# Kernel optimization log

Hardware: AMD Instinct MI355X
Metric: run time of the kernel (lower is better)

Reference implementation:

```python
import jax, jax.numpy as jnp
import numpy as np

N = 50000
E_RAND = 800000
IN_DIM, HIDDEN, OUT_DIM, HEADS = 256, 32, 40, 4


def glorot(key, fan_in, fan_out, shape):
    r = np.sqrt(6.0 / (fan_in + fan_out))
    return jax.random.uniform(key, shape, jnp.float32, -r, r)


def setup_inputs() -> dict:
    key = jax.random.key(0)
    ks = jax.random.split(key, 10)
    x = jax.random.normal(ks[0], (N, IN_DIM), jnp.float32)
    # random edges with src != dst, then append self loops (remove+add_self_loops semantics)
    s = jax.random.randint(ks[1], (E_RAND,), 0, N, jnp.int32)
    d = (s + 1 + jax.random.randint(ks[2], (E_RAND,), 0, N - 1, jnp.int32)) % N
    loops = jnp.arange(N, dtype=jnp.int32)
    src = jnp.concatenate([s, loops])
    dst = jnp.concatenate([d, loops])
    lin1 = glorot(ks[3], IN_DIM, HEADS * HIDDEN, (IN_DIM, HEADS * HIDDEN))
    att_q1 = glorot(ks[4], HEADS, HIDDEN, (1, HEADS, HIDDEN))
    att_v1 = glorot(ks[5], HEADS, HIDDEN, (1, HEADS, HIDDEN))
    bias1 = jnp.zeros((HEADS * HIDDEN,), jnp.float32)
    lin2 = glorot(ks[6], HEADS * HIDDEN, HEADS * OUT_DIM, (HEADS * HIDDEN, HEADS * OUT_DIM))
    att_q2 = glorot(ks[7], HEADS, OUT_DIM, (1, HEADS, OUT_DIM))
    att_v2 = glorot(ks[8], HEADS, OUT_DIM, (1, HEADS, OUT_DIM))
    bias2 = jnp.zeros((OUT_DIM,), jnp.float32)
    return {"x": x, "src": src, "dst": dst,
            "lin1": lin1, "att_q1": att_q1, "att_v1": att_v1, "bias1": bias1,
            "lin2": lin2, "att_q2": att_q2, "att_v2": att_v2, "bias2": bias2}


def segment_softmax(e, seg, n):
    # e: [E, H]; softmax grouped by target node seg
    m = jax.ops.segment_max(e, seg, num_segments=n)  # [N, H]
    ex = jnp.exp(e - m[seg])
    s = jax.ops.segment_sum(ex, seg, num_segments=n)
    return ex / (s[seg] + 1e-16)


def ood_gat_conv(x, src, dst, lin, att_q, att_v, bias, concat):
    n = x.shape[0]
    H, C = att_q.shape[1], att_q.shape[2]
    xh = (x @ lin).reshape(n, H, C)                     # [N, H, C]
    alpha = jnp.sum(xh * att_q, axis=-1)                # [N, H]
    sa = jax.nn.sigmoid(alpha)
    w_alpha = 1.0 - jnp.abs(sa[dst] - sa[src])          # [E, H]
    w_beta = jnp.sum(att_v * jax.nn.leaky_relu(xh[dst] + xh[src]), axis=-1)  # [E, H]
    w = segment_softmax(w_alpha * w_beta, dst, n)       # [E, H]
    out = jax.ops.segment_sum(xh[src] * w[..., None], dst, num_segments=n)  # [N, H, C]
    out = out.reshape(n, H * C) if concat else out.mean(axis=1)
    return out + bias


def reference(x, src, dst, lin1, att_q1, att_v1, bias1, lin2, att_q2, att_v2, bias2):
    h = ood_gat_conv(x, src, dst, lin1, att_q1, att_v1, bias1, concat=True)
    h = jax.nn.elu(h)
    out = ood_gat_conv(h, src, dst, lin2, att_q2, att_v2, bias2, concat=False)
    return out
```

## Files before the change

kernel.cpp:

```cpp
#include <hip/hip_runtime.h>
#include <hip/hip_fp16.h>

#define HEADS 4

typedef _Float16 v2h __attribute__((ext_vector_type(2)));

__device__ __forceinline__ float4 ldh4(const __half* p) {
    const uint2 u = *(const uint2*)p;
    const float2 a = __half22float2(*(const __half2*)&u.x);
    const float2 b = __half22float2(*(const __half2*)&u.y);
    return make_float4(a.x, a.y, b.x, b.y);
}

__device__ __forceinline__ __half2 habs2_(__half2 x) {
    unsigned u = *reinterpret_cast<unsigned*>(&x) & 0x7FFF7FFFu;
    return *reinterpret_cast<__half2*>(&u);
}

__device__ __forceinline__ float fdot2_(__half2 a, __half2 b, float c) {
    return __builtin_amdgcn_fdot2(*(v2h*)&a, *(v2h*)&b, c, false);
}

template <int BN, bool AHALF>
__device__ __forceinline__ void gemm_alpha_body(
    const void* __restrict__ Av, const __half2* __restrict__ Bh,
    const float* __restrict__ attq, __half* __restrict__ Cout,
    float* __restrict__ sa, int M, int K, int bid) {
    constexpr int BM = 64, BK = 32;
    constexpr int MN = BN / 16;
    constexpr int C = BN / 4;
    __shared__ v2h As2[BK / 2][BM];
    __shared__ v2h Bs2[BK / 2][BN];
    __shared__ float sred[BM][4];
    __shared__ float aq[BN];
    const int m0 = bid * BM;
    const int tid = threadIdx.x;
    const int ty = tid >> 4;
    const int tx = tid & 15;
    for (int i = tid; i < BN; i += 256) aq[i] = attq[i];
    sred[tid >> 2][tid & 3] = 0.f;
    float acc[4][MN] = {};

    for (int kt = 0; kt < K; kt += BK) {
        if (!AHALF) {
            const float* A = (const float*)Av;
            #pragma unroll
            for (int it = 0; it < 2; ++it) {
                const int i = tid + 256 * it;
                const int row = i >> 3;
                const int kc = (i & 7) * 4;
                const int grow = m0 + row;
                float4 v = make_float4(0.f, 0.f, 0.f, 0.f);
                if (grow < M) v = *(const float4*)&A[(size_t)grow * K + kt + kc];
                v2h p0; p0[0] = (_Float16)v.x; p0[1] = (_Float16)v.y;
                v2h p1; p1[0] = (_Float16)v.z; p1[1] = (_Float16)v.w;
                As2[(kc >> 1) + 0][row] = p0;
                As2[(kc >> 1) + 1][row] = p1;
            }
        } else {
            const __half* A = (const __half*)Av;
            #pragma unroll
            for (int it = 0; it < 2; ++it) {
                const int i = tid + 256 * it;
                const int row = i >> 3;
                const int kc = (i & 7) * 4;
                const int grow = m0 + row;
                uint2 u = make_uint2(0u, 0u);
                if (grow < M) u = *(const uint2*)&A[(size_t)grow * K + kt + kc];
                As2[(kc >> 1) + 0][row] = *(v2h*)&u.x;
                As2[(kc >> 1) + 1][row] = *(v2h*)&u.y;
            }
        }
        {
            constexpr int BCH = (BK / 2) * (BN / 4);
            for (int i = tid; i < BCH; i += 256) {
                const int k2 = i / (BN / 4);
                const int n4 = (i % (BN / 4)) * 4;
                *(float4*)&Bs2[k2][n4] =
                    *(const float4*)&Bh[(size_t)(kt / 2 + k2) * BN + n4];
            }
        }
        __syncthreads();
        #pragma unroll
        for (int k2 = 0; k2 < BK / 2; ++k2) {
            v2h a_[4], b_[MN];
            #pragma unroll
            for (int i = 0; i < 4; ++i) a_[i] = As2[k2][ty * 4 + i];
            #pragma unroll
            for (int j = 0; j < MN; ++j) b_[j] = Bs2[k2][tx * MN + j];
            #pragma unroll
            for (int i = 0; i < 4; ++i)
                #pragma unroll
                for (int j = 0; j < MN; ++j)
                    acc[i][j] = __builtin_amdgcn_fdot2(a_[i], b_[j], acc[i][j], false);
        }
        __syncthreads();
    }
    const int cbase = tx * MN;
    const int head = cbase / C;
    #pragma unroll
    for (int i = 0; i < 4; ++i) {
        const int grow = m0 + ty * 4 + i;
        if (grow < M) {
            #pragma unroll
            for (int j = 0; j < MN; j += 2) {
                const __half2 h = __floats2half2_rn(acc[i][j], acc[i][j + 1]);
                *(__half2*)&Cout[(size_t)grow * BN + cbase + j] = h;
            }
            float part = 0.f;
            #pragma unroll
            for (int j = 0; j < MN; ++j) part += acc[i][j] * aq[cbase + j];
            atomicAdd(&sred[ty * 4 + i][head], part);
        }
    }
    __syncthreads();
    {
        const int row = m0 + (tid >> 2);
        if (row < M)
            sa[row * 4 + (tid & 3)] =
                1.0f / (1.0f + __expf(-sred[tid >> 2][tid & 3]));
    }
}

__global__ __launch_bounds__(256)
void prep_k(const float* __restrict__ lin1, const float* __restrict__ lin2,
            __half2* __restrict__ l1h, __half2* __restrict__ l2h,
            const int* __restrict__ dst, int* __restrict__ deg,
            int CVB, int E) {
    if ((int)blockIdx.x < CVB) {
        const int t = blockIdx.x * 256 + threadIdx.x;
        if (t < 128 * 128) {
            const int k2 = t >> 7, nn = t & 127;
            l1h[t] = __floats2half2_rn(lin1[(2 * k2) * 128 + nn],
                                       lin1[(2 * k2 + 1) * 128 + nn]);
        } else {
            const int u = t - 128 * 128;
            if (u < 64 * 160) {
                const int k2 = u / 160, nn = u % 160;
                l2h[u] = __floats2half2_rn(lin2[(2 * k2) * 160 + nn],
                                           lin2[(2 * k2 + 1) * 160 + nn]);
            }
        }
    } else {
        const int e = ((int)blockIdx.x - CVB) * 256 + threadIdx.x;
        if (e < E) atomicAdd(&deg[dst[e]], 1);
    }
}

__global__ __launch_bounds__(256)
void scan1_k(const int* __restrict__ deg, int* __restrict__ ro,
             int* __restrict__ bsum, int n) {
    __shared__ int s[256];
    int i = blockIdx.x * 256 + threadIdx.x;
    int v = (i < n) ? deg[i] : 0;
    s[threadIdx.x] = v;
    __syncthreads();
    for (int off = 1; off < 256; off <<= 1) {
        int t = (threadIdx.x >= off) ? s[threadIdx.x - off] : 0;
        __syncthreads();
        s[threadIdx.x] += t;
        __syncthreads();
    }
    if (i < n) ro[i] = s[threadIdx.x] - v;
    if (threadIdx.x == 255) bsum[blockIdx.x] = s[255];
}

__global__ __launch_bounds__(256)
void scan23_k(int* __restrict__ ro, int* __restrict__ cur,
              const int* __restrict__ bsum, int n, int E, int nb) {
    __shared__ int s[256];
    int v = ((int)threadIdx.x < nb) ? bsum[threadIdx.x] : 0;
    s[threadIdx.x] = v;
    __syncthreads();
    for (int off = 1; off < 256; off <<= 1) {
        int t = (threadIdx.x >= off) ? s[threadIdx.x - off] : 0;
        __syncthreads();
        s[threadIdx.x] += t;
        __syncthreads();
    }
    const int pref = (blockIdx.x == 0) ? 0 : s[blockIdx.x - 1];
    const int i = blockIdx.x * 256 + threadIdx.x;
    if (i < n) {
        const int r = ro[i] + pref;
        ro[i] = r;
        cur[i] = r;
    }
    if (i == 0) ro[n] = E;
}

__global__ __launch_bounds__(256)
void front2_k(const float* __restrict__ x, const __half2* __restrict__ l1h,
              const float* __restrict__ attq1, __half* __restrict__ xh,
              float* __restrict__ sa, const int* __restrict__ src,
              const int* __restrict__ dst, int* __restrict__ cur,
              int* __restrict__ csr_src, int M, int K, int MB, int E) {
    if ((int)blockIdx.x < MB) {
        gemm_alpha_body<128, false>(x, l1h, attq1, xh, sa, M, K, blockIdx.x);
    } else {
        const int e = ((int)blockIdx.x - MB) * 256 + threadIdx.x;
        if (e < E) {
            const int d = dst[e];
            const int pos = atomicAdd(&cur[d], 1);
            csr_src[pos] = src[e];
        }
    }
}

__global__ __launch_bounds__(256)
void gemm2_k(const __half* __restrict__ acc16, const __half2* __restrict__ l2h,
             const float* __restrict__ attq2, __half* __restrict__ xh,
             float* __restrict__ sa, int M, int K) {
    gemm_alpha_body<160, true>(acc16, l2h, attq2, xh, sa, M, K, blockIdx.x);
}

template <int C, bool CONCAT>
__global__ __launch_bounds__(256)
void fused_edge_k(const int* __restrict__ ro, const int* __restrict__ csr_src,
                  const __half* __restrict__ xh, const float* __restrict__ sa,
                  const float* __restrict__ attv, const float* __restrict__ bias,
                  void* __restrict__ outp, int n) {
    constexpr int HC = 4 * C;
    constexpr int QH = C / 4;
    constexpr int CHUNK = 64;
    constexpr bool DUAL = (C <= 32);
    const int wid = threadIdx.x >> 6;
    const int lane = threadIdx.x & 63;
    const int node = blockIdx.x * 4 + wid;

    __shared__ float wbuf[4][CHUNK * 4];
    __shared__ int sibuf[4][CHUNK];
    __shared__ __half2 avs[HC / 2];
    for (int i = threadIdx.x; i < HC / 2; i += 256)
        avs[i] = __floats2half2_rn(attv[2 * i], attv[2 * i + 1]);
    __syncthreads();
    if (node >= n) return;

    const int s0 = ro[node], s1 = ro[node + 1];

    const int e_loc = lane >> 2;
    const int h_l = lane & 3;
    const float sad = sa[node * 4 + h_l];
    const __half2 c505 = __floats2half2_rn(0.505f, 0.505f);
    const __half2 c495 = __floats2half2_rn(0.495f, 0.495f);

    __half2 xd[QH * 2];
    {
        const __half* p = &xh[(size_t)node * HC + h_l * C];
        #pragma unroll
        for (int i = 0; i < QH; ++i) {
            const uint2 u = *(const uint2*)&p[i * 4];
            xd[2 * i] = *(const __half2*)&u.x;
            xd[2 * i + 1] = *(const __half2*)&u.y;
        }
    }

    const int half_ = DUAL ? (lane >> 5) : 0;
    const int q = DUAL ? (lane & 31) : lane;
    const int h_a = (q < C) ? (q / QH) : 0;

    float4 acc = make_float4(0.f, 0.f, 0.f, 0.f);
    float ssum = 0.f;

    for (int base = s0; base < s1; base += CHUNK) {
        const int cnt = min(CHUNK, s1 - base);
        const int npass = (cnt + 15) >> 4;
        for (int p = 0; p < npass; ++p) {
            const int eidx = p * 16 + e_loc;
            const int j = base + eidx;
            float w = 0.f;
            int si = 0;
            if (j < s1) {
                si = csr_src[j];
                const float sas = sa[si * 4 + h_l];
                const float wa = 1.0f - fabsf(sad - sas);
                const __half* xs = &xh[(size_t)si * HC + h_l * C];
                float wb = 0.f;
                #pragma unroll
                for (int i = 0; i < QH; ++i) {
                    const uint2 u = *(const uint2*)&xs[i * 4];
                    const __half2 a0 = *(const __half2*)&u.x;
                    const __half2 a1 = *(const __half2*)&u.y;
                    const __half2 t0 = __hadd2(a0, xd[2 * i]);
                    const __half2 t1 = __hadd2(a1, xd[2 * i + 1]);
                    const __half2 l0 = __hfma2(t0, c505, __hmul2(habs2_(t0), c495));
                    const __half2 l1 = __hfma2(t1, c505, __hmul2(habs2_(t1), c495));
                    wb = fdot2_(l0, avs[h_l * QH * 2 + 2 * i], wb);
                    wb = fdot2_(l1, avs[h_l * QH * 2 + 2 * i + 1], wb);
                }
                w = __expf(fminf(wa * wb, 60.f));
                ssum += w;
            }
            wbuf[wid][eidx * 4 + h_l] = w;
            if (h_l == 0) sibuf[wid][eidx] = si;
        }
        const int padded = npass << 4;
        if (q < C) {
            if (DUAL) {
                for (int i = 0; i < padded; i += 8) {
                    const int e0 = i + half_, e1 = i + half_ + 2;
                    const int e2 = i + half_ + 4, e3 = i + half_ + 6;
                    const int i0 = sibuf[wid][e0], i1 = sibuf[wid][e1];
                    const int i2 = sibuf[wid][e2], i3 = sibuf[wid][e3];
                    const float w0 = wbuf[wid][e0 * 4 + h_a];
                    const float w1 = wbuf[wid][e1 * 4 + h_a];
                    const float w2 = wbuf[wid][e2 * 4 + h_a];
                    const float w3 = wbuf[wid][e3 * 4 + h_a];
                    const float4 v0 = ldh4(&xh[(size_t)i0 * HC + q * 4]);
                    const float4 v1 = ldh4(&xh[(size_t)i1 * HC + q * 4]);
                    const float4 v2 = ldh4(&xh[(size_t)i2 * HC + q * 4]);
                    const float4 v3 = ldh4(&xh[(size_t)i3 * HC + q * 4]);
                    acc.x += w0 * v0.x + w1 * v1.x + w2 * v2.x + w3 * v3.x;
                    acc.y += w0 * v0.y + w1 * v1.y + w2 * v2.y + w3 * v3.y;
                    acc.z += w0 * v0.z + w1 * v1.z + w2 * v2.z + w3 * v3.z;
                    acc.w += w0 * v0.w + w1 * v1.w + w2 * v2.w + w3 * v3.w;
                }
            } else {
                for (int i = 0; i < padded; i += 4) {
                    const int i0 = sibuf[wid][i],     i1 = sibuf[wid][i + 1];
                    const int i2 = sibuf[wid][i + 2], i3 = sibuf[wid][i + 3];
                    const float w0 = wbuf[wid][(i + 0) * 4 + h_a];
                    const float w1 = wbuf[wid][(i + 1) * 4 + h_a];
                    const float w2 = wbuf[wid][(i + 2) * 4 + h_a];
                    const float w3 = wbuf[wid][(i + 3) * 4 + h_a];
                    const float4 v0 = ldh4(&xh[(size_t)i0 * HC + q * 4]);
                    const float4 v1 = ldh4(&xh[(size_t)i1 * HC + q * 4]);
                    const float4 v2 = ldh4(&xh[(size_t)i2 * HC + q * 4]);
                    const float4 v3 = ldh4(&xh[(size_t)i3 * HC + q * 4]);
                    acc.x += w0 * v0.x + w1 * v1.x + w2 * v2.x + w3 * v3.x;
                    acc.y += w0 * v0.y + w1 * v1.y + w2 * v2.y + w3 * v3.y;
                    acc.z += w0 * v0.z + w1 * v1.z + w2 * v2.z + w3 * v3.z;
                    acc.w += w0 * v0.w + w1 * v1.w + w2 * v2.w + w3 * v3.w;
                }
            }
        }
    }

    if (DUAL) {
        acc.x += __shfl_xor(acc.x, 32, 64);
        acc.y += __shfl_xor(acc.y, 32, 64);
        acc.z += __shfl_xor(acc.z, 32, 64);
        acc.w += __shfl_xor(acc.w, 32, 64);
    }

    #pragma unroll
    for (int off = 4; off < 64; off <<= 1) ssum += __shfl_xor(ssum, off, 64);
    const float stot = __shfl(ssum, h_a, 64);
    const float inv = 1.0f / (stot + 1e-20f);
    acc.x *= inv; acc.y *= inv; acc.z *= inv; acc.w *= inv;

    if (CONCAT) {
        if (q < C && half_ == 0) {
            const float4 b = ((const float4*)bias)[q];
            float4 v = make_float4(acc.x + b.x, acc.y + b.y, acc.z + b.z, acc.w + b.w);
            v.x = v.x > 0.f ? v.x : __expf(v.x) - 1.0f;
            v.y = v.y > 0.f ? v.y : __expf(v.y) - 1.0f;
            v.z = v.z > 0.f ? v.z : __expf(v.z) - 1.0f;
            v.w = v.w > 0.f ? v.w : __expf(v.w) - 1.0f;
            __half* o16 = (__half*)outp;
            const __half2 h01 = __floats2half2_rn(v.x, v.y);
            const __half2 h23 = __floats2half2_rn(v.z, v.w);
            uint2 u;
            u.x = *(const unsigned*)&h01;
            u.y = *(const unsigned*)&h23;
            *(uint2*)&o16[(size_t)node * HC + q * 4] = u;
        }
    } else {
        const int qq = (q < QH) ? q : 0;
        const float x1 = __shfl(acc.x, qq + QH, 64);
        const float y1 = __shfl(acc.y, qq + QH, 64);
        const float z1 = __shfl(acc.z, qq + QH, 64);
        const float w1 = __shfl(acc.w, qq + QH, 64);
        const float x2 = __shfl(acc.x, qq + 2 * QH, 64);
        const float y2 = __shfl(acc.y, qq + 2 * QH, 64);
        const float z2 = __shfl(acc.z, qq + 2 * QH, 64);
        const float w2 = __shfl(acc.w, qq + 2 * QH, 64);
        const float x3 = __shfl(acc.x, qq + 3 * QH, 64);
        const float y3 = __shfl(acc.y, qq + 3 * QH, 64);
        const float z3 = __shfl(acc.z, qq + 3 * QH, 64);
        const float w3 = __shfl(acc.w, qq + 3 * QH, 64);
        if (q < QH && half_ == 0) {
            float* of = (float*)outp;
            const float4 b = ((const float4*)bias)[q];
            float4 v;
            v.x = 0.25f * (acc.x + x1 + x2 + x3) + b.x;
            v.y = 0.25f * (acc.y + y1 + y2 + y3) + b.y;
            v.z = 0.25f * (acc.z + z1 + z2 + z3) + b.z;
            v.w = 0.25f * (acc.w + w1 + w2 + w3) + b.w;
            *(float4*)&of[(size_t)node * C + q * 4] = v;
        }
    }
}

extern "C" void kernel_launch(void* const* d_in, const int* in_sizes, int n_in,
                              void* d_out, int out_size, void* d_ws, size_t ws_size,
                              hipStream_t stream) {
    const float* x      = (const float*)d_in[0];
    const int*   src    = (const int*)d_in[1];
    const int*   dst    = (const int*)d_in[2];
    const float* lin1   = (const float*)d_in[3];
    const float* att_q1 = (const float*)d_in[4];
    const float* att_v1 = (const float*)d_in[5];
    const float* bias1  = (const float*)d_in[6];
    const float* lin2   = (const float*)d_in[7];
    const float* att_q2 = (const float*)d_in[8];
    const float* att_v2 = (const float*)d_in[9];
    const float* bias2  = (const float*)d_in[10];
    float* outp = (float*)d_out;

    const int n = in_sizes[0] / 256;
    const int E = in_sizes[1];
    const int nh = n * HEADS;
    const int NB = (n + 255) / 256;

    char* wsb = (char*)d_ws;
    size_t o = 0;
    __half* xh     = (__half*)(wsb + o); o += (size_t)n * 160 * 2;
    __half* acc16  = (__half*)(wsb + o); o += (size_t)n * 128 * 2;
    float* sa      = (float*)(wsb + o); o += (size_t)nh * 4;
    int* csr_src   = (int*)(wsb + o); o += (size_t)E * 4;
    int* deg       = (int*)(wsb + o); o += (size_t)n * 4;
    int* ro        = (int*)(wsb + o); o += (size_t)(n + 1) * 4;
    int* cur       = (int*)(wsb + o); o += (size_t)n * 4;
    int* bsum      = (int*)(wsb + o); o += 256 * 4;
    __half2* l1h   = (__half2*)(wsb + o); o += (size_t)128 * 128 * 4;
    __half2* l2h   = (__half2*)(wsb + o); o += (size_t)64 * 160 * 4;

    dim3 blk(256);
    const int EG = (E + 255) / 256;
    const int MB = (n + 63) / 64;
    const int CVB = (128 * 128 + 64 * 160 + 255) / 256;

    hipMemsetAsync(deg, 0, (size_t)n * 4, stream);
    prep_k<<<CVB + EG, blk, 0, stream>>>(lin1, lin2, l1h, l2h, dst, deg, CVB, E);
    scan1_k<<<NB, blk, 0, stream>>>(deg, ro, bsum, n);
    scan23_k<<<NB, blk, 0, stream>>>(ro, cur, bsum, n, E, NB);
    front2_k<<<MB + EG, blk, 0, stream>>>(x, l1h, att_q1, xh, sa, src, dst,
                                          cur, csr_src, n, 256, MB, E);
    fused_edge_k<32, true><<<(n + 3) / 4, blk, 0, stream>>>(ro, csr_src, xh, sa, att_v1, bias1, acc16, n);
    gemm2_k<<<MB, blk, 0, stream>>>(acc16, l2h, att_q2, xh, sa, n, 128);
    fused_edge_k<40, false><<<(n + 3) / 4, blk, 0, stream>>>(ro, csr_src, xh, sa, att_v2, bias2, outp, n);
}
```

Measured before the change: 320.2 us.

## Use MFMA 16x16x32 f16 instructions for both linear-layer GEMMs

Replaces the fdot2-based register-tiled GEMM with wave-level MFMA 16x16x32 f16 instructions. Each wave computes a 16-row strip across all output columns. The weights are now pre-transposed into K-contiguous half layout, and A/B tiles are stored in padded LDS rows. The epilogue writes fp16 outputs per element and reduces the attention dot products via LDS atomics. This aims to cut the compute time of the two dense projections, at the cost of scalar half stores and more atomics in the epilogue.

```diff
diff --git a/kernel.cpp b/kernel.cpp
--- a/kernel.cpp
+++ b/kernel.cpp
@@ -4,6 +4,8 @@
 #define HEADS 4
 
 typedef _Float16 v2h __attribute__((ext_vector_type(2)));
+typedef _Float16 v8h __attribute__((ext_vector_type(8)));
+typedef float v4f __attribute__((ext_vector_type(4)));
 
 __device__ __forceinline__ float4 ldh4(const __half* p) {
     const uint2 u = *(const uint2*)p;
@@ -23,94 +25,85 @@
 
 template <int BN, bool AHALF>
 __device__ __forceinline__ void gemm_alpha_body(
-    const void* __restrict__ Av, const __half2* __restrict__ Bh,
+    const void* __restrict__ Av, const _Float16* __restrict__ BT,
     const float* __restrict__ attq, __half* __restrict__ Cout,
     float* __restrict__ sa, int M, int K, int bid) {
-    constexpr int BM = 64, BK = 32;
-    constexpr int MN = BN / 16;
+    constexpr int NT = BN / 16;
     constexpr int C = BN / 4;
-    __shared__ v2h As2[BK / 2][BM];
-    __shared__ v2h Bs2[BK / 2][BN];
-    __shared__ float sred[BM][4];
+    constexpr int APAD = 40;
+    __shared__ _Float16 As[64 * APAD];
+    __shared__ _Float16 Bs[BN * APAD];
     __shared__ float aq[BN];
-    const int m0 = bid * BM;
+    __shared__ float sred[64][4];
+    const int m0 = bid * 64;
     const int tid = threadIdx.x;
-    const int ty = tid >> 4;
-    const int tx = tid & 15;
+    const int wave = tid >> 6;
+    const int lane = tid & 63;
+    const int l15 = lane & 15;
+    const int kg = lane >> 4;
+
     for (int i = tid; i < BN; i += 256) aq[i] = attq[i];
     sred[tid >> 2][tid & 3] = 0.f;
-    float acc[4][MN] = {};
-
-    for (int kt = 0; kt < K; kt += BK) {
-        if (!AHALF) {
-            const float* A = (const float*)Av;
+
+    v4f acc[NT];
+    #pragma unroll
+    for (int ct = 0; ct < NT; ++ct) acc[ct] = (v4f){0.f, 0.f, 0.f, 0.f};
+
+    for (int kt = 0; kt < K; kt += 32) {
+        {
+            const int row = tid >> 2;
+            const int seg = (tid & 3) * 8;
+            const int grow = m0 + row;
+            v8h hv = (v8h){0, 0, 0, 0, 0, 0, 0, 0};
+            if (grow < M) {
+                if (!AHALF) {
+                    const float* A = (const float*)Av;
+                    const float4 f0 = *(const float4*)&A[(size_t)grow * K + kt + seg];
+                    const float4 f1 = *(const float4*)&A[(size_t)grow * K + kt + seg + 4];
+                    hv[0] = (_Float16)f0.x; hv[1] = (_Float16)f0.y;
+                    hv[2] = (_Float16)f0.z; hv[3] = (_Float16)f0.w;
+                    hv[4] = (_Float16)f1.x; hv[5] = (_Float16)f1.y;
+                    hv[6] = (_Float16)f1.z; hv[7] = (_Float16)f1.w;
+                } else {
+                    const _Float16* A = (const _Float16*)Av;
+                    hv = *(const v8h*)&A[(size_t)grow * K + kt + seg];
+                }
+            }
+            *(v8h*)&As[row * APAD + seg] = hv;
+        }
+        for (int i = tid; i < BN * 4; i += 256) {
+            const int rowb = i >> 2;
+            const int seg = (i & 3) * 8;
+            *(v8h*)&Bs[rowb * APAD + seg] =
+                *(const v8h*)&BT[(size_t)rowb * K + kt + seg];
+        }
+        __syncthreads();
+        {
+            const v8h a = *(const v8h*)&As[(wave * 16 + l15) * APAD + kg * 8];
             #pragma unroll
-            for (int it = 0; it < 2; ++it) {
-                const int i = tid + 256 * it;
-                const int row = i >> 3;
-                const int kc = (i & 7) * 4;
-                const int grow = m0 + row;
-                float4 v = make_float4(0.f, 0.f, 0.f, 0.f);
-                if (grow < M) v = *(const float4*)&A[(size_t)grow * K + kt + kc];
-                v2h p0; p0[0] = (_Float16)v.x; p0[1] = (_Float16)v.y;
-                v2h p1; p1[0] = (_Float16)v.z; p1[1] = (_Float16)v.w;
-                As2[(kc >> 1) + 0][row] = p0;
-                As2[(kc >> 1) + 1][row] = p1;
-            }
-        } else {
-            const __half* A = (const __half*)Av;
+            for (int ct = 0; ct < NT; ++ct) {
+                const v8h b = *(const v8h*)&Bs[(ct * 16 + l15) * APAD + kg * 8];
+                acc[ct] = __builtin_amdgcn_mfma_f32_16x16x32_f16(a, b, acc[ct], 0, 0, 0);
+            }
+        }
+        __syncthreads();
+    }
+    #pragma unroll
+    for (int reg = 0; reg < 4; ++reg) {
+        const int rloc = wave * 16 + kg * 4 + reg;
+        const int grow = m0 + rloc;
+        if (grow < M) {
+            float hacc[4] = {0.f, 0.f, 0.f, 0.f};
             #pragma unroll
-            for (int it = 0; it < 2; ++it) {
-                const int i = tid + 256 * it;
-                const int row = i >> 3;
-                const int kc = (i & 7) * 4;
-                const int grow = m0 + row;
-                uint2 u = make_uint2(0u, 0u);
-                if (grow < M) u = *(const uint2*)&A[(size_t)grow * K + kt + kc];
-                As2[(kc >> 1) + 0][row] = *(v2h*)&u.x;
-                As2[(kc >> 1) + 1][row] = *(v2h*)&u.y;
-            }
-        }
-        {
-            constexpr int BCH = (BK / 2) * (BN / 4);
-            for (int i = tid; i < BCH; i += 256) {
-                const int k2 = i / (BN / 4);
-                const int n4 = (i % (BN / 4)) * 4;
-                *(float4*)&Bs2[k2][n4] =
-                    *(const float4*)&Bh[(size_t)(kt / 2 + k2) * BN + n4];
-            }
-        }
-        __syncthreads();
-        #pragma unroll
-        for (int k2 = 0; k2 < BK / 2; ++k2) {
-            v2h a_[4], b_[MN];
+            for (int ct = 0; ct < NT; ++ct) {
+                const int col = ct * 16 + l15;
+                const float v = acc[ct][reg];
+                Cout[(size_t)grow * BN + col] = (__half)v;
+                hacc[col / C] += v * aq[col];
+            }
             #pragma unroll
-            for (int i = 0; i < 4; ++i) a_[i] = As2[k2][ty * 4 + i];
-            #pragma unroll
-            for (int j = 0; j < MN; ++j) b_[j] = Bs2[k2][tx * MN + j];
-            #pragma unroll
-            for (int i = 0; i < 4; ++i)
-                #pragma unroll
-                for (int j = 0; j < MN; ++j)
-                    acc[i][j] = __builtin_amdgcn_fdot2(a_[i], b_[j], acc[i][j], false);
-        }
-        __syncthreads();
-    }
-    const int cbase = tx * MN;
-    const int head = cbase / C;
-    #pragma unroll
-    for (int i = 0; i < 4; ++i) {
-        const int grow = m0 + ty * 4 + i;
-        if (grow < M) {
-            #pragma unroll
-            for (int j = 0; j < MN; j += 2) {
-                const __half2 h = __floats2half2_rn(acc[i][j], acc[i][j + 1]);
-                *(__half2*)&Cout[(size_t)grow * BN + cbase + j] = h;
-            }
-            float part = 0.f;
-            #pragma unroll
-            for (int j = 0; j < MN; ++j) part += acc[i][j] * aq[cbase + j];
-            atomicAdd(&sred[ty * 4 + i][head], part);
+            for (int h = 0; h < 4; ++h)
+                if (hacc[h] != 0.f) atomicAdd(&sred[rloc][h], hacc[h]);
         }
     }
     __syncthreads();
@@ -124,21 +117,19 @@
 
 __global__ __launch_bounds__(256)
 void prep_k(const float* __restrict__ lin1, const float* __restrict__ lin2,
-            __half2* __restrict__ l1h, __half2* __restrict__ l2h,
+            _Float16* __restrict__ l1T, _Float16* __restrict__ l2T,
             const int* __restrict__ dst, int* __restrict__ deg,
             int CVB, int E) {
     if ((int)blockIdx.x < CVB) {
         const int t = blockIdx.x * 256 + threadIdx.x;
-        if (t < 128 * 128) {
-            const int k2 = t >> 7, nn = t & 127;
-            l1h[t] = __floats2half2_rn(lin1[(2 * k2) * 128 + nn],
-                                       lin1[(2 * k2 + 1) * 128 + nn]);
+        if (t < 128 * 256) {
+            const int nn = t >> 8, k = t & 255;
+            l1T[t] = (_Float16)lin1[(size_t)k * 128 + nn];
         } else {
-            const int u = t - 128 * 128;
-            if (u < 64 * 160) {
-                const int k2 = u / 160, nn = u % 160;
-                l2h[u] = __floats2half2_rn(lin2[(2 * k2) * 160 + nn],
-                                           lin2[(2 * k2 + 1) * 160 + nn]);
+            const int u = t - 128 * 256;
+            if (u < 160 * 128) {
+                const int nn = u >> 7, k = u & 127;
+                l2T[u] = (_Float16)lin2[(size_t)k * 160 + nn];
             }
         }
     } else {
@@ -189,13 +180,13 @@
 }
 
 __global__ __launch_bounds__(256)
-void front2_k(const float* __restrict__ x, const __half2* __restrict__ l1h,
+void front2_k(const float* __restrict__ x, const _Float16* __restrict__ l1T,
               const float* __restrict__ attq1, __half* __restrict__ xh,
               float* __restrict__ sa, const int* __restrict__ src,
               const int* __restrict__ dst, int* __restrict__ cur,
               int* __restrict__ csr_src, int M, int K, int MB, int E) {
     if ((int)blockIdx.x < MB) {
-        gemm_alpha_body<128, false>(x, l1h, attq1, xh, sa, M, K, blockIdx.x);
+        gemm_alpha_body<128, false>(x, l1T, attq1, xh, sa, M, K, blockIdx.x);
     } else {
         const int e = ((int)blockIdx.x - MB) * 256 + threadIdx.x;
         if (e < E) {
@@ -207,10 +198,10 @@
 }
 
 __global__ __launch_bounds__(256)
-void gemm2_k(const __half* __restrict__ acc16, const __half2* __restrict__ l2h,
+void gemm2_k(const __half* __restrict__ acc16, const _Float16* __restrict__ l2T,
              const float* __restrict__ attq2, __half* __restrict__ xh,
              float* __restrict__ sa, int M, int K) {
-    gemm_alpha_body<160, true>(acc16, l2h, attq2, xh, sa, M, K, blockIdx.x);
+    gemm_alpha_body<160, true>(acc16, l2T, attq2, xh, sa, M, K, blockIdx.x);
 }
 
 template <int C, bool CONCAT>
@@ -422,21 +413,21 @@
     int* ro        = (int*)(wsb + o); o += (size_t)(n + 1) * 4;
     int* cur       = (int*)(wsb + o); o += (size_t)n * 4;
     int* bsum      = (int*)(wsb + o); o += 256 * 4;
-    __half2* l1h   = (__half2*)(wsb + o); o += (size_t)128 * 128 * 4;
-    __half2* l2h   = (__half2*)(wsb + o); o += (size_t)64 * 160 * 4;
+    _Float16* l1T  = (_Float16*)(wsb + o); o += (size_t)128 * 256 * 2;
+    _Float16* l2T  = (_Float16*)(wsb + o); o += (size_t)160 * 128 * 2;
 
     dim3 blk(256);
     const int EG = (E + 255) / 256;
     const int MB = (n + 63) / 64;
-    const int CVB = (128 * 128 + 64 * 160 + 255) / 256;
+    const int CVB = (128 * 256 + 160 * 128 + 255) / 256;
 
     hipMemsetAsync(deg, 0, (size_t)n * 4, stream);
-    prep_k<<<CVB + EG, blk, 0, stream>>>(lin1, lin2, l1h, l2h, dst, deg, CVB, E);
+    prep_k<<<CVB + EG, blk, 0, stream>>>(lin1, lin2, l1T, l2T, dst, deg, CVB, E);
     scan1_k<<<NB, blk, 0, stream>>>(deg, ro, bsum, n);
     scan23_k<<<NB, blk, 0, stream>>>(ro, cur, bsum, n, E, NB);
-    front2_k<<<MB + EG, blk, 0, stream>>>(x, l1h, att_q1, xh, sa, src, dst,
+    front2_k<<<MB + EG, blk, 0, stream>>>(x, l1T, att_q1, xh, sa, src, dst,
                                           cur, csr_src, n, 256, MB, E);
     fused_edge_k<32, true><<<(n + 3) / 4, blk, 0, stream>>>(ro, csr_src, xh, sa, att_v1, bias1, acc16, n);
-    gemm2_k<<<MB, blk, 0, stream>>>(acc16, l2h, att_q2, xh, sa, n, 128);
+    gemm2_k<<<MB, blk, 0, stream>>>(acc16, l2T, att_q2, xh, sa, n, 128);
     fused_edge_k<40, false><<<(n + 3) / 4, blk, 0, stream>>>(ro, csr_src, xh, sa, att_v2, bias2, outp, n);
 }
```

New measurement: 323.5 us. No clear change (+1.0%).
